# Kernel optimization log

Hardware: AMD Instinct MI355X
Metric: run time of the kernel (lower is better)

The kernel has to match this reference:

```python
import jax, jax.numpy as jnp
import numpy as np

OUT_FEATS = 4096
IN_FEATS = 16384
EPS = 1e-8


def setup_inputs() -> dict:
    key = jax.random.key(0)
    k1, k2 = jax.random.split(key)
    raw_update = jax.random.normal(k1, (OUT_FEATS, IN_FEATS), dtype=jnp.float32)
    # v initialized as in the module: randn * 0.001
    v = jax.random.normal(k2, (OUT_FEATS,), dtype=jnp.float32) * 0.001
    return {"raw_update": raw_update, "v": v}


def reference(raw_update, v):
    # Faithful to: raw_update - (v v^T / (||v||^2 + eps)) @ raw_update
    # Efficient form: GEMV then rank-1 broadcast subtract, O(n*m) instead of O(n^2*m).
    denom = jnp.sum(v * v) + EPS            # ||v||^2 + eps (scalar)
    coeff = (v @ raw_update) / denom         # [in_feats]
    return raw_update - v[:, None] * coeff[None, :]
```

## Files before the change

kernel.cpp:

```cpp
#include <hip/hip_runtime.h>
#include <cstddef>

typedef float f4 __attribute__((ext_vector_type(4)));

#define OUT_FEATS 4096
#define IN_FEATS  16384
#define NCOL4     (IN_FEATS / 4)
#define EPS       1e-8f

#define BT   256
#define SW8  8
#define NBLK (NCOL4 / SW8)
#define RG   (BT / SW8)
#define KPT  (OUT_FEATS / RG)

__global__ void __launch_bounds__(BT)
k_fused(const f4* __restrict__ A4,
        const float* __restrict__ v,
        f4* __restrict__ out) {
    __shared__ float vs[OUT_FEATS];
    __shared__ f4    red[BT];
    __shared__ float dred[4];
    __shared__ f4    cfl[SW8];

    const int T = threadIdx.x;
    const int q = T & (SW8 - 1);
    const int g = T >> 3;
    const int c4 = blockIdx.x * SW8 + q;

    float vsq = 0.f;
    {
        const f4* v4 = (const f4*)v;
        #pragma unroll
        for (int i = 0; i < OUT_FEATS / 4 / BT; ++i) {
            const f4 x = v4[T + i * BT];
            ((f4*)vs)[T + i * BT] = x;
            vsq += x.x * x.x + x.y * x.y + x.z * x.z + x.w * x.w;
        }
    }
    #pragma unroll
    for (int off = 32; off > 0; off >>= 1) vsq += __shfl_down(vsq, off, 64);
    if ((T & 63) == 0) dred[T >> 6] = vsq;
    __syncthreads();
    const float denom = dred[0] + dred[1] + dred[2] + dred[3] + EPS;

    f4 acc[8];
    #pragma unroll
    for (int u = 0; u < 8; ++u) acc[u] = 0.f;

    const size_t base = (size_t)g * NCOL4 + c4;
    for (int k = 0; k < KPT; k += 8) {
        f4 a[8];
        #pragma unroll
        for (int u = 0; u < 8; ++u)
            a[u] = A4[base + (size_t)(k + u) * RG * NCOL4];
        #pragma unroll
        for (int u = 0; u < 8; ++u)
            acc[u] += vs[g + (k + u) * RG] * a[u];
    }
    const f4 s = ((acc[0] + acc[1]) + (acc[2] + acc[3])) +
                 ((acc[4] + acc[5]) + (acc[6] + acc[7]));

    red[T] = s;
    __syncthreads();
    #pragma unroll
    for (int s2 = RG / 2; s2 >= 1; s2 >>= 1) {
        if (g < s2) red[T] += red[T + s2 * SW8];
        __syncthreads();
    }
    if (T < SW8) cfl[T] = red[T] / denom;
    __syncthreads();
    const f4 cf = cfl[q];

    for (int k = KPT - 8; k >= 0; k -= 8) {
        f4 a[8];
        #pragma unroll
        for (int u = 0; u < 8; ++u)
            a[u] = A4[base + (size_t)(k + 7 - u) * RG * NCOL4];
        #pragma unroll
        for (int u = 0; u < 8; ++u) {
            const int kk = k + 7 - u;
            const f4 o = a[u] - vs[g + kk * RG] * cf;
            __builtin_nontemporal_store(o, &out[base + (size_t)kk * RG * NCOL4]);
        }
    }
}

extern "C" void kernel_launch(void* const* d_in, const int* in_sizes, int n_in,
                              void* d_out, int out_size, void* d_ws, size_t ws_size,
                              hipStream_t stream) {
    const f4*    A4 = (const f4*)d_in[0];
    const float* v  = (const float*)d_in[1];
    f4* out = (f4*)d_out;

    k_fused<<<NBLK, BT, 0, stream>>>(A4, v, out);
}
```

Baseline: 117.7 us.

## Double-buffer A loads in both passes and use shuffle-based column reduction

Adds register double-buffering (pa/pb) so the next 8-row chunk of A is loaded while the current one is being accumulated or written. The first chunks are issued before the v-norm computation, and the last chunks of the GEMV pass are reused at the start of the write pass. The shared-memory tree reduction, which had several barriers, becomes wave shuffles plus one barrier. This aims to hide memory latency and cut synchronisation. In exchange it raises register pressure, which may lower occupancy.

New measurement: 116.0 us (median of 2 runs). About the same (-1.5%).

```diff
diff --git a/kernel.cpp b/kernel.cpp
--- a/kernel.cpp
+++ b/kernel.cpp
@@ -19,14 +19,23 @@
         const float* __restrict__ v,
         f4* __restrict__ out) {
     __shared__ float vs[OUT_FEATS];
-    __shared__ f4    red[BT];
+    __shared__ f4    red[32];
     __shared__ float dred[4];
-    __shared__ f4    cfl[SW8];
 
     const int T = threadIdx.x;
     const int q = T & (SW8 - 1);
     const int g = T >> 3;
+    const int w = T >> 6;
     const int c4 = blockIdx.x * SW8 + q;
+
+    const size_t base = (size_t)g * NCOL4 + c4;
+#define ROWOFF(k) (base + (size_t)(k) * RG * NCOL4)
+
+    f4 pa[8], pb[8];
+    #pragma unroll
+    for (int u = 0; u < 8; ++u) pa[u] = A4[ROWOFF(u)];
+    #pragma unroll
+    for (int u = 0; u < 8; ++u) pb[u] = A4[ROWOFF(8 + u)];
 
     float vsq = 0.f;
     {
@@ -40,7 +49,7 @@
     }
     #pragma unroll
     for (int off = 32; off > 0; off >>= 1) vsq += __shfl_down(vsq, off, 64);
-    if ((T & 63) == 0) dred[T >> 6] = vsq;
+    if ((T & 63) == 0) dred[w] = vsq;
     __syncthreads();
     const float denom = dred[0] + dred[1] + dred[2] + dred[3] + EPS;
 
@@ -48,42 +57,61 @@
     #pragma unroll
     for (int u = 0; u < 8; ++u) acc[u] = 0.f;
 
-    const size_t base = (size_t)g * NCOL4 + c4;
-    for (int k = 0; k < KPT; k += 8) {
-        f4 a[8];
+    #pragma unroll
+    for (int k = 0; k < KPT; k += 16) {
         #pragma unroll
         for (int u = 0; u < 8; ++u)
-            a[u] = A4[base + (size_t)(k + u) * RG * NCOL4];
+            acc[u] += vs[g + (k + u) * RG] * pa[u];
+        if (k + 16 < KPT) {
+            #pragma unroll
+            for (int u = 0; u < 8; ++u) pa[u] = A4[ROWOFF(k + 16 + u)];
+        }
         #pragma unroll
         for (int u = 0; u < 8; ++u)
-            acc[u] += vs[g + (k + u) * RG] * a[u];
+            acc[u] += vs[g + (k + 8 + u) * RG] * pb[u];
+        if (k + 24 < KPT) {
+            #pragma unroll
+            for (int u = 0; u < 8; ++u) pb[u] = A4[ROWOFF(k + 24 + u)];
+        }
     }
-    const f4 s = ((acc[0] + acc[1]) + (acc[2] + acc[3])) +
-                 ((acc[4] + acc[5]) + (acc[6] + acc[7]));
+    f4 s = ((acc[0] + acc[1]) + (acc[2] + acc[3])) +
+           ((acc[4] + acc[5]) + (acc[6] + acc[7]));
 
-    red[T] = s;
+    #pragma unroll
+    for (int off = 8; off <= 32; off <<= 1) {
+        s.x += __shfl_xor(s.x, off, 64);
+        s.y += __shfl_xor(s.y, off, 64);
+        s.z += __shfl_xor(s.z, off, 64);
+        s.w += __shfl_xor(s.w, off, 64);
+    }
+    if ((T & 63) < 8) red[w * 8 + (T & 7)] = s;
     __syncthreads();
+    const f4 cf = (red[q] + red[q + 8] + red[q + 16] + red[q + 24]) / denom;
+
     #pragma unroll
-    for (int s2 = RG / 2; s2 >= 1; s2 >>= 1) {
-        if (g < s2) red[T] += red[T + s2 * SW8];
-        __syncthreads();
-    }
-    if (T < SW8) cfl[T] = red[T] / denom;
-    __syncthreads();
-    const f4 cf = cfl[q];
-
-    for (int k = KPT - 8; k >= 0; k -= 8) {
-        f4 a[8];
-        #pragma unroll
-        for (int u = 0; u < 8; ++u)
-            a[u] = A4[base + (size_t)(k + 7 - u) * RG * NCOL4];
+    for (int k = KPT - 8; k >= 8; k -= 16) {
         #pragma unroll
         for (int u = 0; u < 8; ++u) {
-            const int kk = k + 7 - u;
-            const f4 o = a[u] - vs[g + kk * RG] * cf;
-            __builtin_nontemporal_store(o, &out[base + (size_t)kk * RG * NCOL4]);
+            const int kk = k + u;
+            __builtin_nontemporal_store(pb[u] - vs[g + kk * RG] * cf,
+                                        &out[ROWOFF(kk)]);
+        }
+        if (k - 16 >= 0) {
+            #pragma unroll
+            for (int u = 0; u < 8; ++u) pb[u] = A4[ROWOFF(k - 16 + u)];
+        }
+        #pragma unroll
+        for (int u = 0; u < 8; ++u) {
+            const int kk = k - 8 + u;
+            __builtin_nontemporal_store(pa[u] - vs[g + kk * RG] * cf,
+                                        &out[ROWOFF(kk)]);
+        }
+        if (k - 24 >= 0) {
+            #pragma unroll
+            for (int u = 0; u < 8; ++u) pa[u] = A4[ROWOFF(k - 24 + u)];
         }
     }
+#undef ROWOFF
 }
 
 extern "C" void kernel_launch(void* const* d_in, const int* in_sizes, int n_in,
```
